# Performance work log

Hardware: AMD Instinct MI355X
Metric: run time of the kernel (lower is better)

The kernel has to match this reference:

```python
import jax, jax.numpy as jnp
import numpy as np

N = 100000       # nodes
E = 1600000      # undirected edges (one direction stored)
D = 64           # feature_dim


def _linear_params(key, fan_in, fan_out):
    kw, kb = jax.random.split(key)
    s = 1.0 / np.sqrt(fan_in)
    W = jax.random.uniform(kw, (fan_in, fan_out), jnp.float32, -s, s)
    b = jax.random.uniform(kb, (fan_out,), jnp.float32, -s, s)
    return W, b


def setup_inputs() -> dict:
    key = jax.random.key(0)
    ks = jax.random.split(key, 8)
    node_features = jax.random.normal(ks[0], (N, D), jnp.float32)
    node_operations = jax.random.normal(ks[1], (N, 4), jnp.float32)

    # Unique undirected edges, no self-loops -> torch's set() dedup of
    # {outgoing} U {incoming} neighbors equals counting each stored edge once
    # in both directions.
    rng = np.random.default_rng(0)
    src = rng.integers(0, N, size=4 * E)
    dst = rng.integers(0, N, size=4 * E)
    lo, hi = np.minimum(src, dst), np.maximum(src, dst)
    keep = lo != hi
    pairs = np.unique(np.stack([lo[keep], hi[keep]], axis=1), axis=0)
    assert pairs.shape[0] >= E
    perm = rng.permutation(pairs.shape[0])[:E]
    edge_index = jnp.asarray(pairs[perm].T, dtype=jnp.int32)  # [2, E]

    # node_generator: Linear(2D,128)-ReLU-Linear(128,64)-ReLU-Linear(64,D+3)
    W1, b1 = _linear_params(ks[2], 2 * D, 128)
    W2, b2 = _linear_params(ks[3], 128, 64)
    W3, b3 = _linear_params(ks[4], 64, D + 3)
    # insertion_predictor: Linear(D,32)-ReLU-Linear(32,1)-Sigmoid
    P1, pb1 = _linear_params(ks[5], D, 32)
    P2, pb2 = _linear_params(ks[6], 32, 1)

    return {
        'node_features': node_features,
        'node_operations': node_operations,
        'edge_index': edge_index,
        'W1': W1, 'b1': b1, 'W2': W2, 'b2': b2, 'W3': W3, 'b3': b3,
        'P1': P1, 'pb1': pb1, 'P2': P2, 'pb2': pb2,
    }


def reference(node_features, node_operations, edge_index,
              W1, b1, W2, b2, W3, b3, P1, pb1, P2, pb2):
    n = node_features.shape[0]
    src, dst = edge_index[0], edge_index[1]

    # candidate mask: softmax over op logits, class 0 = insert, threshold 0.5
    insert_probs = jax.nn.softmax(node_operations, axis=-1)[:, 0]
    ones = jnp.ones(src.shape[0], node_features.dtype)
    deg = (jax.ops.segment_sum(ones, src, num_segments=n)
           + jax.ops.segment_sum(ones, dst, num_segments=n))
    # torch loop skips candidates with no neighbors
    mask = (insert_probs > 0.5) & (deg > 0)
    maskf = mask.astype(node_features.dtype)

    # batched neighbor mean (undirected: both edge directions)
    nsum = (jax.ops.segment_sum(node_features[dst], src, num_segments=n)
            + jax.ops.segment_sum(node_features[src], dst, num_segments=n))
    nmean = nsum / jnp.maximum(deg, 1.0)[:, None]

    ctx = jnp.concatenate([node_features, nmean], axis=-1)  # [N, 2D]
    h = jax.nn.relu(ctx @ W1 + b1)
    h = jax.nn.relu(h @ W2 + b2)
    gen = h @ W3 + b3                         # [N, D+3]
    pos = gen[:, :3]                          # [N, 3]
    feats = gen[:, 3:]                        # [N, D]
    p = jax.nn.relu(feats @ P1 + pb1)
    prob = jax.nn.sigmoid(p @ P2 + pb2)       # [N, 1]

    # pack: [positions | features | probability], zeroed for non-candidates
    out = jnp.concatenate([pos, feats, prob], axis=-1) * maskf[:, None]
    return out
```

## Files before the change

### kernel.cpp

```cpp
#include <hip/hip_runtime.h>
#include <hip/hip_bf16.h>
#include <hip/hip_fp16.h>
#include <math.h>

typedef unsigned int u32;
typedef unsigned short u16;
typedef unsigned long long u64;

#define O_W1 0
#define O_b1 16384
#define O_W2 16512
#define O_b2 24704
#define O_W3 24768
#define O_b3 29056
#define O_P1 29123
#define O_pb1 31171
#define O_P2 31203
#define O_pb2 31235
#define W_TOTAL 31236

#define NPB 16
#define LDW 17

__device__ __forceinline__ float ldf(const void* p, long i, int dt) {
  if (dt == 1) { u32 v = ((const u16*)p)[i]; return __uint_as_float(v << 16); }
  if (dt == 2) { __half h = ((const __half*)p)[i]; return __half2float(h); }
  return ((const float*)p)[i];
}
__device__ __forceinline__ int ldei(const int* p, long i, int is64) {
  return is64 ? p[2 * i] : p[i];
}
__device__ __forceinline__ int bit_test(const u64* bits, int i) {
  return (int)((bits[i >> 6] >> (i & 63)) & 1ull);
}

extern "C" __global__ void kall_detect(const u32* __restrict__ feat,
                                       const u32* __restrict__ w1,
                                       const u32* __restrict__ ops,
                                       const u32* __restrict__ ei,
                                       int* __restrict__ hdr)
{
  int lane = threadIdx.x;
  int mode = blockIdx.x;
  if (mode == 3) {
    unsigned long long m0 = __ballot(ei[lane] == 0u);
    unsigned long long m1 = __ballot(ei[64 + lane] == 0u);
    if (lane == 0) hdr[2] = (__popcll(m0) + __popcll(m1) >= 32) ? 1 : 0;
    return;
  }
  const u32* p = (mode == 0) ? feat : (mode == 1) ? w1 : ops;
  int slot = (mode == 0) ? 0 : (mode == 1) ? 1 : 3;
  u32 w0 = p[lane];
  u32 w1v = p[64 + lane];
  u16 h[4] = { (u16)(w0 & 0xffff), (u16)(w0 >> 16),
               (u16)(w1v & 0xffff), (u16)(w1v >> 16) };
  int cb = 0;
#pragma unroll
  for (int t = 0; t < 4; ++t) {
    int e8 = (h[t] >> 7) & 0xff;
    cb += (e8 >= 110 && e8 <= 140) ? 1 : 0;
  }
  int ch = 0;
#pragma unroll
  for (int t = 0; t < 4; t += 2) {
    int e5 = (h[t] >> 10) & 0x1f;
    ch += (e5 >= 5 && e5 <= 18) ? 1 : 0;
  }
  __shared__ int sb[64], sh[64];
  sb[lane] = cb; sh[lane] = ch;
  __syncthreads();
  if (lane == 0) {
    int CB = 0, CH = 0;
    for (int t = 0; t < 64; ++t) { CB += sb[t]; CH += sh[t]; }
    int dt;
    if (CB >= 200) dt = 1;
    else if (CH >= 100) dt = 2;
    else dt = 0;
    hdr[slot] = dt;
  }
}

extern "C" __global__ void __launch_bounds__(256)
kw_conv(const void* __restrict__ W1, const void* __restrict__ b1,
        const void* __restrict__ W2, const void* __restrict__ b2,
        const void* __restrict__ W3, const void* __restrict__ b3,
        const void* __restrict__ P1, const void* __restrict__ pb1,
        const void* __restrict__ P2, const void* __restrict__ pb2,
        const int* __restrict__ hdr, float* __restrict__ wf)
{
  int i = blockIdx.x * 256 + threadIdx.x;
  if (i >= W_TOTAL) return;
  const void* s; int o;
  if      (i < O_b1)  { s = W1;  o = i; }
  else if (i < O_W2)  { s = b1;  o = i - O_b1; }
  else if (i < O_b2)  { s = W2;  o = i - O_W2; }
  else if (i < O_W3)  { s = b2;  o = i - O_b2; }
  else if (i < O_b3)  { s = W3;  o = i - O_W3; }
  else if (i < O_P1)  { s = b3;  o = i - O_b3; }
  else if (i < O_pb1) { s = P1;  o = i - O_P1; }
  else if (i < O_P2)  { s = pb1; o = i - O_pb1; }
  else if (i < O_pb2) { s = P2;  o = i - O_P2; }
  else                { s = pb2; o = i - O_pb2; }
  wf[i] = ldf(s, o, hdr[1]);
}

extern "C" __global__ void __launch_bounds__(256)
k2a_cand(const void* __restrict__ opsv, const int* __restrict__ hdr,
         u64* __restrict__ bits, int* __restrict__ cnt,
         int* __restrict__ fillcnt, int N)
{
  int i = blockIdx.x * 256 + threadIdx.x;
  if (i >= N) return;
  cnt[i] = 0;
  fillcnt[i] = 0;
  int dt = hdr[3];
  float x0 = ldf(opsv, (long)i * 4 + 0, dt);
  float x1 = ldf(opsv, (long)i * 4 + 1, dt);
  float x2 = ldf(opsv, (long)i * 4 + 2, dt);
  float x3 = ldf(opsv, (long)i * 4 + 3, dt);
  float m = fmaxf(fmaxf(x0, x1), fmaxf(x2, x3));
  double e0 = exp((double)(x0 - m));
  double e1 = exp((double)(x1 - m));
  double e2 = exp((double)(x2 - m));
  double e3 = exp((double)(x3 - m));
  double p0 = e0 / (((e0 + e1) + e2) + e3);
  u64 msk = __ballot(p0 > 0.5);
  if ((threadIdx.x & 63) == 0) bits[i >> 6] = msk;
}

extern "C" __global__ void __launch_bounds__(256)
k1a_cnt(const int* __restrict__ ei, const u64* __restrict__ bits,
        int* __restrict__ cnt, int E, const int* __restrict__ hdr)
{
  int e = blockIdx.x * 256 + threadIdx.x;
  if (e >= E) return;
  int is64 = hdr[2];
  int s = ldei(ei, e, is64);
  int d = ldei(ei, (long)E + e, is64);
  if (bit_test(bits, s)) atomicAdd(cnt + s, 1);
  if (bit_test(bits, d)) atomicAdd(cnt + d, 1);
}

extern "C" __global__ void __launch_bounds__(256)
k2b_alloc(const u64* __restrict__ bits, const int* __restrict__ cnt,
          int* __restrict__ hdr, int* __restrict__ nodeoff,
          int* __restrict__ nlist, int N)
{
  int i = blockIdx.x * 256 + threadIdx.x;
  if (i >= N) return;
  int c = (bit_test(bits, i) && cnt[i] > 0) ? cnt[i] : 0;
  if (c > 0) {
    int pos = atomicAdd(hdr + 4, 1);
    nlist[pos] = i;
    nodeoff[i] = atomicAdd(hdr + 5, c);
  } else {
    nodeoff[i] = -1;
  }
}

extern "C" __global__ void __launch_bounds__(256)
k1_fill(const int* __restrict__ ei, const u64* __restrict__ bits,
        const int* __restrict__ nodeoff,
        int* __restrict__ fillcnt, int* __restrict__ adj, int E,
        const int* __restrict__ hdr)
{
  int e = blockIdx.x * 256 + threadIdx.x;
  if (e >= E) return;
  int is64 = hdr[2];
  int s = ldei(ei, e, is64);
  int d = ldei(ei, (long)E + e, is64);
  if (bit_test(bits, s)) {
    int os = nodeoff[s];
    if (os >= 0) { int p = atomicAdd(fillcnt + s, 1); adj[os + p] = d; }
  }
  if (bit_test(bits, d)) {
    int od = nodeoff[d];
    if (od >= 0) { int p = atomicAdd(fillcnt + d, 1); adj[od + p] = s; }
  }
}

extern "C" __global__ void __launch_bounds__(256)
k3b_mlp(const void* __restrict__ featv, const int* __restrict__ nlist,
        const int* __restrict__ cnt, const int* __restrict__ nodeoff,
        const int* __restrict__ adj,
        const float* __restrict__ wf, const int* __restrict__ hdr,
        float* __restrict__ out)
{
  __shared__ float A[128 * LDW];
  __shared__ float B[128 * LDW];
  __shared__ float WS[4096];
  __shared__ int sNode[NPB];
  __shared__ int sDeg[NPB];
  __shared__ int sOff[NPB];
  const int tid = threadIdx.x;
  const int nmask = hdr[4];
  const int base = blockIdx.x * NPB;
  if (nmask == 0 || base >= nmask) return;
  const int dt = hdr[0];
  const int nl = tid & 15;
  const int jg = tid >> 4;
  const int lane = tid & 63;
  const int q = __builtin_amdgcn_readfirstlane(tid >> 6);

  if (tid < NPB) {
    int idx = base + tid;
    int node = nlist[(idx < nmask) ? idx : (nmask - 1)];
    sNode[tid] = node;
    sDeg[tid] = cnt[node];
    sOff[tid] = nodeoff[node];
  }
  __syncthreads();

#pragma unroll
  for (int i = 0; i < 4; ++i) {
    int g = i * 256 + tid;
    int f = g & 63;
    int n = g >> 6;
    int node = sNode[n];
    A[f * LDW + n] = ldf(featv, (long)node * 64 + f, dt);
  }

  if (dt == 0) {
    const float4* f4 = (const float4*)featv;
    const int g = lane >> 4;
    const int fq = lane & 15;
#pragma unroll
    for (int t = 0; t < 4; ++t) {
      const int n = q * 4 + t;
      const int off = sOff[n];
      const int dg = sDeg[n];
      float4 acc = make_float4(0.f, 0.f, 0.f, 0.f);
      int j = g;
      for (; j + 4 < dg; j += 8) {
        int n0 = adj[off + j];
        int n1 = adj[off + j + 4];
        float4 v0 = f4[(long)n0 * 16 + fq];
        float4 v1 = f4[(long)n1 * 16 + fq];
        acc.x += v0.x + v1.x; acc.y += v0.y + v1.y;
        acc.z += v0.z + v1.z; acc.w += v0.w + v1.w;
      }
      if (j < dg) {
        int n0 = adj[off + j];
        float4 v0 = f4[(long)n0 * 16 + fq];
        acc.x += v0.x; acc.y += v0.y; acc.z += v0.z; acc.w += v0.w;
      }
      acc.x += __shfl_xor(acc.x, 16); acc.y += __shfl_xor(acc.y, 16);
      acc.z += __shfl_xor(acc.z, 16); acc.w += __shfl_xor(acc.w, 16);
      acc.x += __shfl_xor(acc.x, 32); acc.y += __shfl_xor(acc.y, 32);
      acc.z += __shfl_xor(acc.z, 32); acc.w += __shfl_xor(acc.w, 32);
      if (g == 0) {
        float inv = 1.f / (float)dg;
        A[(64 + fq * 4 + 0) * LDW + n] = acc.x * inv;
        A[(64 + fq * 4 + 1) * LDW + n] = acc.y * inv;
        A[(64 + fq * 4 + 2) * LDW + n] = acc.z * inv;
        A[(64 + fq * 4 + 3) * LDW + n] = acc.w * inv;
      }
    }
  } else {
#pragma unroll
    for (int t = 0; t < 4; ++t) {
      const int n = q * 4 + t;
      const int off = sOff[n];
      const int dg = sDeg[n];
      float acc = 0.f;
      int j = 0;
      for (; j + 4 <= dg; j += 4) {
        int n0 = adj[off + j + 0];
        int n1 = adj[off + j + 1];
        int n2 = adj[off + j + 2];
        int n3 = adj[off + j + 3];
        float v0 = ldf(featv, (long)n0 * 64 + lane, dt);
        float v1 = ldf(featv, (long)n1 * 64 + lane, dt);
        float v2 = ldf(featv, (long)n2 * 64 + lane, dt);
        float v3 = ldf(featv, (long)n3 * 64 + lane, dt);
        acc += ((v0 + v1) + (v2 + v3));
      }
      for (; j < dg; ++j)
        acc += ldf(featv, (long)adj[off + j] * 64 + lane, dt);
      A[(64 + lane) * LDW + n] = acc / (float)dg;
    }
  }

  {
    const int j0 = jg * 8;
    float a0 = wf[O_b1 + j0 + 0], a1 = wf[O_b1 + j0 + 1];
    float a2 = wf[O_b1 + j0 + 2], a3 = wf[O_b1 + j0 + 3];
    float a4 = wf[O_b1 + j0 + 4], a5 = wf[O_b1 + j0 + 5];
    float a6 = wf[O_b1 + j0 + 6], a7 = wf[O_b1 + j0 + 7];
    for (int c = 0; c < 4; ++c) {
      __syncthreads();
      {
        const float4* s4 = (const float4*)(wf + O_W1 + c * 4096);
        float4* d4 = (float4*)WS;
#pragma unroll
        for (int i = 0; i < 4; ++i) d4[tid + 256 * i] = s4[tid + 256 * i];
      }
      __syncthreads();
#pragma unroll 4
      for (int k = 0; k < 32; ++k) {
        float x = A[(c * 32 + k) * LDW + nl];
        const float* w = WS + k * 128 + j0;
        float4 w0 = *(const float4*)(w);
        float4 w1 = *(const float4*)(w + 4);
        a0 = fmaf(x, w0.x, a0);
        a1 = fmaf(x, w0.y, a1);
        a2 = fmaf(x, w0.z, a2);
        a3 = fmaf(x, w0.w, a3);
        a4 = fmaf(x, w1.x, a4);
        a5 = fmaf(x, w1.y, a5);
        a6 = fmaf(x, w1.z, a6);
        a7 = fmaf(x, w1.w, a7);
      }
    }
    B[(j0 + 0) * LDW + nl] = fmaxf(a0, 0.f);
    B[(j0 + 1) * LDW + nl] = fmaxf(a1, 0.f);
    B[(j0 + 2) * LDW + nl] = fmaxf(a2, 0.f);
    B[(j0 + 3) * LDW + nl] = fmaxf(a3, 0.f);
    B[(j0 + 4) * LDW + nl] = fmaxf(a4, 0.f);
    B[(j0 + 5) * LDW + nl] = fmaxf(a5, 0.f);
    B[(j0 + 6) * LDW + nl] = fmaxf(a6, 0.f);
    B[(j0 + 7) * LDW + nl] = fmaxf(a7, 0.f);
  }

  {
    const int j0 = jg * 4;
    float a0 = wf[O_b2 + j0 + 0], a1 = wf[O_b2 + j0 + 1];
    float a2 = wf[O_b2 + j0 + 2], a3 = wf[O_b2 + j0 + 3];
    for (int c = 0; c < 2; ++c) {
      __syncthreads();
      {
        const float4* s4 = (const float4*)(wf + O_W2 + c * 4096);
        float4* d4 = (float4*)WS;
#pragma unroll
        for (int i = 0; i < 4; ++i) d4[tid + 256 * i] = s4[tid + 256 * i];
      }
      __syncthreads();
#pragma unroll 4
      for (int k = 0; k < 64; ++k) {
        float x = B[(c * 64 + k) * LDW + nl];
        float4 w = *(const float4*)(WS + k * 64 + j0);
        a0 = fmaf(x, w.x, a0);
        a1 = fmaf(x, w.y, a1);
        a2 = fmaf(x, w.z, a2);
        a3 = fmaf(x, w.w, a3);
      }
    }
    A[(j0 + 0) * LDW + nl] = fmaxf(a0, 0.f);
    A[(j0 + 1) * LDW + nl] = fmaxf(a1, 0.f);
    A[(j0 + 2) * LDW + nl] = fmaxf(a2, 0.f);
    A[(j0 + 3) * LDW + nl] = fmaxf(a3, 0.f);
  }

  {
    const int jq = jg;
    const bool has5 = (jq < 3);
    float a0 = 0.f, a1 = 0.f, a2 = 0.f, a3 = 0.f, a4 = 0.f;
    for (int c = 0; c < 2; ++c) {
      __syncthreads();
      {
        const float4* s4 = (const float4*)(wf + O_W3 + c * 2144);
        float4* d4 = (float4*)WS;
        for (int i = tid; i < 536; i += 256) d4[i] = s4[i];
      }
      __syncthreads();
#pragma unroll 4
      for (int k = 0; k < 32; ++k) {
        float x = A[(c * 32 + k) * LDW + nl];
        const float* w = WS + k * 67 + jq;
        float w4 = has5 ? w[64] : 0.f;
        a0 = fmaf(x, w[0],  a0);
        a1 = fmaf(x, w[16], a1);
        a2 = fmaf(x, w[32], a2);
        a3 = fmaf(x, w[48], a3);
        a4 = fmaf(x, w4,    a4);
      }
    }
    B[(jq +  0) * LDW + nl] = wf[O_b3 + jq]      + a0;
    B[(jq + 16) * LDW + nl] = wf[O_b3 + jq + 16] + a1;
    B[(jq + 32) * LDW + nl] = wf[O_b3 + jq + 32] + a2;
    B[(jq + 48) * LDW + nl] = wf[O_b3 + jq + 48] + a3;
    if (has5)
      B[(jq + 64) * LDW + nl] = wf[O_b3 + jq + 64] + a4;
  }

  {
    const int jq = jg;
    float a0 = wf[O_pb1 + jq], a1 = wf[O_pb1 + jq + 16];
    __syncthreads();
    for (int i = tid; i < 2048; i += 256) WS[i] = wf[O_P1 + i];
    __syncthreads();
#pragma unroll 4
    for (int k = 0; k < 64; ++k) {
      float x = B[(3 + k) * LDW + nl];
      a0 = fmaf(x, WS[k * 32 + jq],      a0);
      a1 = fmaf(x, WS[k * 32 + jq + 16], a1);
    }
    A[(jq +  0) * LDW + nl] = fmaxf(a0, 0.f);
    A[(jq + 16) * LDW + nl] = fmaxf(a1, 0.f);
  }
  __syncthreads();

  if (tid < 64) {
    const int part = tid >> 4;
    float p = 0.f;
#pragma unroll
    for (int kk = 0; kk < 8; ++kk) {
      int k = part * 8 + kk;
      p = fmaf(A[k * LDW + nl], wf[O_P2 + k], p);
    }
    p += __shfl_xor(p, 16);
    p += __shfl_xor(p, 32);
    if (part == 0) {
      float z = wf[O_pb2] + p;
      B[67 * LDW + nl] = 1.0f / (1.0f + expf(-z));
    }
  }
  __syncthreads();

  for (int g = tid; g < NPB * 68; g += 256) {
    int n = g / 68;
    int c = g - n * 68;
    if (base + n < nmask) {
      int node = sNode[n];
      out[(long)node * 68 + c] = B[c * LDW + n];
    }
  }
}

extern "C" void kernel_launch(void* const* d_in, const int* in_sizes, int n_in,
                              void* d_out, int out_size, void* d_ws, size_t ws_size,
                              hipStream_t stream) {
  int iF = 0, iO = 1, iE = 2;
  int iW1 = 3, ib1 = 4, iW2 = 5, ib2 = 6, iW3 = 7, ib3 = 8;
  int iP1 = 9, ipb1 = 10, iP2 = 11, ipb2 = 12;
  {
    int bigs[4]; int nb = 0;
    for (int i = 0; i < n_in && nb < 4; ++i)
      if (in_sizes[i] > 100000) bigs[nb++] = i;
    if (nb == 3) {
      int a = bigs[0], b = bigs[1], c = bigs[2];
      int mx = a, mn = a;
      if (in_sizes[b] > in_sizes[mx]) mx = b;
      if (in_sizes[c] > in_sizes[mx]) mx = c;
      if (in_sizes[b] < in_sizes[mn]) mn = b;
      if (in_sizes[c] < in_sizes[mn]) mn = c;
      iF = mx; iO = mn; iE = a + b + c - mx - mn;
      int t32[2]; int n32 = 0;
      int jW1=-1, jb1=-1, jW2=-1, jb2=-1, jW3=-1, jb3=-1, jP1=-1, jpb2=-1;
      for (int i = 0; i < n_in; ++i) {
        if (i == iF || i == iO || i == iE) continue;
        switch (in_sizes[i]) {
          case 16384: jW1 = i; break;
          case 128:   jb1 = i; break;
          case 8192:  jW2 = i; break;
          case 64:    jb2 = i; break;
          case 4288:  jW3 = i; break;
          case 67:    jb3 = i; break;
          case 2048:  jP1 = i; break;
          case 1:     jpb2 = i; break;
          case 32:    if (n32 < 2) t32[n32++] = i; break;
          default: break;
        }
      }
      if (jW1 >= 0 && jb1 >= 0 && jW2 >= 0 && jb2 >= 0 && jW3 >= 0 &&
          jb3 >= 0 && jP1 >= 0 && jpb2 >= 0 && n32 == 2) {
        iW1 = jW1; ib1 = jb1; iW2 = jW2; ib2 = jb2; iW3 = jW3; ib3 = jb3;
        iP1 = jP1; ipb2 = jpb2;
        if (t32[1] == t32[0] + 1) { ipb1 = t32[0]; iP2 = t32[1]; }
        else                      { iP2 = t32[0]; ipb1 = t32[1]; }
      }
    }
  }
  int N = (out_size % 68 == 0) ? (out_size / 68) : (in_sizes[iF] / 64);
  const int E = in_sizes[iE] / 2;
  const void* feat = d_in[iF];
  const void* ops  = d_in[iO];
  const int* ei    = (const int*)d_in[iE];

  char* ws = (char*)d_ws;
  int* hdr = (int*)ws;
  size_t off = 256;
  float* wf = (float*)(ws + off);
  off += ((size_t)W_TOTAL * 4 + 255) & ~(size_t)255;
  u64* bits = (u64*)(ws + off);
  off += (((size_t)(N + 63) / 64) * 8 + 255) & ~(size_t)255;
  int* cnt = (int*)(ws + off);
  off += ((size_t)N * 4 + 255) & ~(size_t)255;
  int* nodeoff = (int*)(ws + off);
  off += ((size_t)N * 4 + 255) & ~(size_t)255;
  int* fillcnt = (int*)(ws + off);
  off += ((size_t)N * 4 + 255) & ~(size_t)255;
  int* nlist = (int*)(ws + off);
  off += ((size_t)N * 4 + 255) & ~(size_t)255;
  int* adj = (int*)(ws + off);

  hipMemsetAsync(hdr, 0, 256, stream);
  hipMemsetAsync(d_out, 0, (size_t)out_size * 4, stream);

  kall_detect<<<4, 64, 0, stream>>>((const u32*)feat, (const u32*)d_in[iW1],
                                    (const u32*)ops, (const u32*)ei, hdr);

  kw_conv<<<(W_TOTAL + 255) / 256, 256, 0, stream>>>(
      d_in[iW1], d_in[ib1], d_in[iW2], d_in[ib2], d_in[iW3], d_in[ib3],
      d_in[iP1], d_in[ipb1], d_in[iP2], d_in[ipb2], hdr, wf);
  k2a_cand<<<(N + 255) / 256, 256, 0, stream>>>(ops, hdr, bits, cnt, fillcnt, N);
  k1a_cnt<<<(E + 255) / 256, 256, 0, stream>>>(ei, bits, cnt, E, hdr);
  k2b_alloc<<<(N + 255) / 256, 256, 0, stream>>>(bits, cnt, hdr, nodeoff, nlist, N);
  k1_fill<<<(E + 255) / 256, 256, 0, stream>>>(ei, bits, nodeoff, fillcnt, adj, E, hdr);
  k3b_mlp<<<(N + NPB - 1) / NPB, 256, 0, stream>>>(feat, nlist, cnt, nodeoff,
                                                   adj, wf, hdr,
                                                   (float*)d_out);
}
```

Baseline: 241.2 us.

## Halve MLP nodes per block, vectorize edge kernels, use cursor-based CSR fill

The MLP kernel now processes 8 candidate nodes per block instead of 16, which doubles the block count and shrinks per-thread accumulators for more parallelism and occupancy. The price is more weight reloads into shared memory overall. The edge count and fill kernels now handle 4 edges per thread with int4 loads. The fill kernel uses a cursor array initialized to each node's start offset, which removes the nodeoff lookup and the add in the inner path.

Result: no change. 245.3 us (+1.7%).

```diff
diff --git a/kernel.cpp b/kernel.cpp
--- a/kernel.cpp
+++ b/kernel.cpp
@@ -19,8 +19,8 @@
 #define O_pb2 31235
 #define W_TOTAL 31236
 
-#define NPB 16
-#define LDW 17
+#define NPB 8
+#define LDW 9
 
 __device__ __forceinline__ float ldf(const void* p, long i, int dt) {
   if (dt == 1) { u32 v = ((const u16*)p)[i]; return __uint_as_float(v << 16); }
@@ -106,13 +106,11 @@
 
 extern "C" __global__ void __launch_bounds__(256)
 k2a_cand(const void* __restrict__ opsv, const int* __restrict__ hdr,
-         u64* __restrict__ bits, int* __restrict__ cnt,
-         int* __restrict__ fillcnt, int N)
+         u64* __restrict__ bits, int* __restrict__ cnt, int N)
 {
   int i = blockIdx.x * 256 + threadIdx.x;
   if (i >= N) return;
   cnt[i] = 0;
-  fillcnt[i] = 0;
   int dt = hdr[3];
   float x0 = ldf(opsv, (long)i * 4 + 0, dt);
   float x1 = ldf(opsv, (long)i * 4 + 1, dt);
@@ -132,19 +130,36 @@
 k1a_cnt(const int* __restrict__ ei, const u64* __restrict__ bits,
         int* __restrict__ cnt, int E, const int* __restrict__ hdr)
 {
-  int e = blockIdx.x * 256 + threadIdx.x;
-  if (e >= E) return;
+  int t = blockIdx.x * 256 + threadIdx.x;
+  int e0 = t * 4;
+  if (e0 >= E) return;
   int is64 = hdr[2];
-  int s = ldei(ei, e, is64);
-  int d = ldei(ei, (long)E + e, is64);
-  if (bit_test(bits, s)) atomicAdd(cnt + s, 1);
-  if (bit_test(bits, d)) atomicAdd(cnt + d, 1);
+  if (!is64 && (E & 3) == 0 && e0 + 4 <= E) {
+    int4 sv = *(const int4*)(ei + e0);
+    int4 dv = *(const int4*)(ei + (long)E + e0);
+    if (bit_test(bits, sv.x)) atomicAdd(cnt + sv.x, 1);
+    if (bit_test(bits, sv.y)) atomicAdd(cnt + sv.y, 1);
+    if (bit_test(bits, sv.z)) atomicAdd(cnt + sv.z, 1);
+    if (bit_test(bits, sv.w)) atomicAdd(cnt + sv.w, 1);
+    if (bit_test(bits, dv.x)) atomicAdd(cnt + dv.x, 1);
+    if (bit_test(bits, dv.y)) atomicAdd(cnt + dv.y, 1);
+    if (bit_test(bits, dv.z)) atomicAdd(cnt + dv.z, 1);
+    if (bit_test(bits, dv.w)) atomicAdd(cnt + dv.w, 1);
+  } else {
+    int ee = (e0 + 4 < E) ? e0 + 4 : E;
+    for (int e = e0; e < ee; ++e) {
+      int s = ldei(ei, e, is64);
+      int d = ldei(ei, (long)E + e, is64);
+      if (bit_test(bits, s)) atomicAdd(cnt + s, 1);
+      if (bit_test(bits, d)) atomicAdd(cnt + d, 1);
+    }
+  }
 }
 
 extern "C" __global__ void __launch_bounds__(256)
 k2b_alloc(const u64* __restrict__ bits, const int* __restrict__ cnt,
           int* __restrict__ hdr, int* __restrict__ nodeoff,
-          int* __restrict__ nlist, int N)
+          int* __restrict__ fillcnt, int* __restrict__ nlist, int N)
 {
   int i = blockIdx.x * 256 + threadIdx.x;
   if (i >= N) return;
@@ -152,7 +167,9 @@
   if (c > 0) {
     int pos = atomicAdd(hdr + 4, 1);
     nlist[pos] = i;
-    nodeoff[i] = atomicAdd(hdr + 5, c);
+    int start = atomicAdd(hdr + 5, c);
+    nodeoff[i] = start;
+    fillcnt[i] = start;
   } else {
     nodeoff[i] = -1;
   }
@@ -160,22 +177,32 @@
 
 extern "C" __global__ void __launch_bounds__(256)
 k1_fill(const int* __restrict__ ei, const u64* __restrict__ bits,
-        const int* __restrict__ nodeoff,
-        int* __restrict__ fillcnt, int* __restrict__ adj, int E,
+        int* __restrict__ cur, int* __restrict__ adj, int E,
         const int* __restrict__ hdr)
 {
-  int e = blockIdx.x * 256 + threadIdx.x;
-  if (e >= E) return;
+  int t = blockIdx.x * 256 + threadIdx.x;
+  int e0 = t * 4;
+  if (e0 >= E) return;
   int is64 = hdr[2];
-  int s = ldei(ei, e, is64);
-  int d = ldei(ei, (long)E + e, is64);
-  if (bit_test(bits, s)) {
-    int os = nodeoff[s];
-    if (os >= 0) { int p = atomicAdd(fillcnt + s, 1); adj[os + p] = d; }
-  }
-  if (bit_test(bits, d)) {
-    int od = nodeoff[d];
-    if (od >= 0) { int p = atomicAdd(fillcnt + d, 1); adj[od + p] = s; }
+  if (!is64 && (E & 3) == 0 && e0 + 4 <= E) {
+    int4 sv = *(const int4*)(ei + e0);
+    int4 dv = *(const int4*)(ei + (long)E + e0);
+    if (bit_test(bits, sv.x)) { int p = atomicAdd(cur + sv.x, 1); adj[p] = dv.x; }
+    if (bit_test(bits, dv.x)) { int p = atomicAdd(cur + dv.x, 1); adj[p] = sv.x; }
+    if (bit_test(bits, sv.y)) { int p = atomicAdd(cur + sv.y, 1); adj[p] = dv.y; }
+    if (bit_test(bits, dv.y)) { int p = atomicAdd(cur + dv.y, 1); adj[p] = sv.y; }
+    if (bit_test(bits, sv.z)) { int p = atomicAdd(cur + sv.z, 1); adj[p] = dv.z; }
+    if (bit_test(bits, dv.z)) { int p = atomicAdd(cur + dv.z, 1); adj[p] = sv.z; }
+    if (bit_test(bits, sv.w)) { int p = atomicAdd(cur + sv.w, 1); adj[p] = dv.w; }
+    if (bit_test(bits, dv.w)) { int p = atomicAdd(cur + dv.w, 1); adj[p] = sv.w; }
+  } else {
+    int ee = (e0 + 4 < E) ? e0 + 4 : E;
+    for (int e = e0; e < ee; ++e) {
+      int s = ldei(ei, e, is64);
+      int d = ldei(ei, (long)E + e, is64);
+      if (bit_test(bits, s)) { int p = atomicAdd(cur + s, 1); adj[p] = d; }
+      if (bit_test(bits, d)) { int p = atomicAdd(cur + d, 1); adj[p] = s; }
+    }
   }
 }
 
@@ -197,8 +224,8 @@
   const int base = blockIdx.x * NPB;
   if (nmask == 0 || base >= nmask) return;
   const int dt = hdr[0];
-  const int nl = tid & 15;
-  const int jg = tid >> 4;
+  const int nl = tid & 7;
+  const int jg = tid >> 3;
   const int lane = tid & 63;
   const int q = __builtin_amdgcn_readfirstlane(tid >> 6);
 
@@ -212,7 +239,7 @@
   __syncthreads();
 
 #pragma unroll
-  for (int i = 0; i < 4; ++i) {
+  for (int i = 0; i < 2; ++i) {
     int g = i * 256 + tid;
     int f = g & 63;
     int n = g >> 6;
@@ -225,8 +252,8 @@
     const int g = lane >> 4;
     const int fq = lane & 15;
 #pragma unroll
-    for (int t = 0; t < 4; ++t) {
-      const int n = q * 4 + t;
+    for (int t = 0; t < 2; ++t) {
+      const int n = q * 2 + t;
       const int off = sOff[n];
       const int dg = sDeg[n];
       float4 acc = make_float4(0.f, 0.f, 0.f, 0.f);
@@ -258,8 +285,8 @@
     }
   } else {
 #pragma unroll
-    for (int t = 0; t < 4; ++t) {
-      const int n = q * 4 + t;
+    for (int t = 0; t < 2; ++t) {
+      const int n = q * 2 + t;
       const int off = sOff[n];
       const int dg = sDeg[n];
       float acc = 0.f;
@@ -282,11 +309,9 @@
   }
 
   {
-    const int j0 = jg * 8;
+    const int j0 = jg * 4;
     float a0 = wf[O_b1 + j0 + 0], a1 = wf[O_b1 + j0 + 1];
     float a2 = wf[O_b1 + j0 + 2], a3 = wf[O_b1 + j0 + 3];
-    float a4 = wf[O_b1 + j0 + 4], a5 = wf[O_b1 + j0 + 5];
-    float a6 = wf[O_b1 + j0 + 6], a7 = wf[O_b1 + j0 + 7];
     for (int c = 0; c < 4; ++c) {
       __syncthreads();
       {
@@ -299,33 +324,22 @@
 #pragma unroll 4
       for (int k = 0; k < 32; ++k) {
         float x = A[(c * 32 + k) * LDW + nl];
-        const float* w = WS + k * 128 + j0;
-        float4 w0 = *(const float4*)(w);
-        float4 w1 = *(const float4*)(w + 4);
-        a0 = fmaf(x, w0.x, a0);
-        a1 = fmaf(x, w0.y, a1);
-        a2 = fmaf(x, w0.z, a2);
-        a3 = fmaf(x, w0.w, a3);
-        a4 = fmaf(x, w1.x, a4);
-        a5 = fmaf(x, w1.y, a5);
-        a6 = fmaf(x, w1.z, a6);
-        a7 = fmaf(x, w1.w, a7);
+        float4 w = *(const float4*)(WS + k * 128 + j0);
+        a0 = fmaf(x, w.x, a0);
+        a1 = fmaf(x, w.y, a1);
+        a2 = fmaf(x, w.z, a2);
+        a3 = fmaf(x, w.w, a3);
       }
     }
     B[(j0 + 0) * LDW + nl] = fmaxf(a0, 0.f);
     B[(j0 + 1) * LDW + nl] = fmaxf(a1, 0.f);
     B[(j0 + 2) * LDW + nl] = fmaxf(a2, 0.f);
     B[(j0 + 3) * LDW + nl] = fmaxf(a3, 0.f);
-    B[(j0 + 4) * LDW + nl] = fmaxf(a4, 0.f);
-    B[(j0 + 5) * LDW + nl] = fmaxf(a5, 0.f);
-    B[(j0 + 6) * LDW + nl] = fmaxf(a6, 0.f);
-    B[(j0 + 7) * LDW + nl] = fmaxf(a7, 0.f);
   }
 
   {
-    const int j0 = jg * 4;
+    const int j0 = jg * 2;
     float a0 = wf[O_b2 + j0 + 0], a1 = wf[O_b2 + j0 + 1];
-    float a2 = wf[O_b2 + j0 + 2], a3 = wf[O_b2 + j0 + 3];
     for (int c = 0; c < 2; ++c) {
       __syncthreads();
       {
@@ -338,23 +352,19 @@
 #pragma unroll 4
       for (int k = 0; k < 64; ++k) {
         float x = B[(c * 64 + k) * LDW + nl];
-        float4 w = *(const float4*)(WS + k * 64 + j0);
+        float2 w = *(const float2*)(WS + k * 64 + j0);
         a0 = fmaf(x, w.x, a0);
         a1 = fmaf(x, w.y, a1);
-        a2 = fmaf(x, w.z, a2);
-        a3 = fmaf(x, w.w, a3);
       }
     }
     A[(j0 + 0) * LDW + nl] = fmaxf(a0, 0.f);
     A[(j0 + 1) * LDW + nl] = fmaxf(a1, 0.f);
-    A[(j0 + 2) * LDW + nl] = fmaxf(a2, 0.f);
-    A[(j0 + 3) * LDW + nl] = fmaxf(a3, 0.f);
   }
 
   {
     const int jq = jg;
-    const bool has5 = (jq < 3);
-    float a0 = 0.f, a1 = 0.f, a2 = 0.f, a3 = 0.f, a4 = 0.f;
+    const bool has3 = (jq < 3);
+    float a0 = 0.f, a1 = 0.f, a2 = 0.f;
     for (int c = 0; c < 2; ++c) {
       __syncthreads();
       {
@@ -367,47 +377,42 @@
       for (int k = 0; k < 32; ++k) {
         float x = A[(c * 32 + k) * LDW + nl];
         const float* w = WS + k * 67 + jq;
-        float w4 = has5 ? w[64] : 0.f;
+        float w2 = has3 ? w[64] : 0.f;
         a0 = fmaf(x, w[0],  a0);
-        a1 = fmaf(x, w[16], a1);
-        a2 = fmaf(x, w[32], a2);
-        a3 = fmaf(x, w[48], a3);
-        a4 = fmaf(x, w4,    a4);
+        a1 = fmaf(x, w[32], a1);
+        a2 = fmaf(x, w2,    a2);
       }
     }
     B[(jq +  0) * LDW + nl] = wf[O_b3 + jq]      + a0;
-    B[(jq + 16) * LDW + nl] = wf[O_b3 + jq + 16] + a1;
-    B[(jq + 32) * LDW + nl] = wf[O_b3 + jq + 32] + a2;
-    B[(jq + 48) * LDW + nl] = wf[O_b3 + jq + 48] + a3;
-    if (has5)
-      B[(jq + 64) * LDW + nl] = wf[O_b3 + jq + 64] + a4;
+    B[(jq + 32) * LDW + nl] = wf[O_b3 + jq + 32] + a1;
+    if (has3)
+      B[(jq + 64) * LDW + nl] = wf[O_b3 + jq + 64] + a2;
   }
 
   {
     const int jq = jg;
-    float a0 = wf[O_pb1 + jq], a1 = wf[O_pb1 + jq + 16];
+    float a0 = wf[O_pb1 + jq];
     __syncthreads();
     for (int i = tid; i < 2048; i += 256) WS[i] = wf[O_P1 + i];
     __syncthreads();
 #pragma unroll 4
     for (int k = 0; k < 64; ++k) {
       float x = B[(3 + k) * LDW + nl];
-      a0 = fmaf(x, WS[k * 32 + jq],      a0);
-      a1 = fmaf(x, WS[k * 32 + jq + 16], a1);
-    }
-    A[(jq +  0) * LDW + nl] = fmaxf(a0, 0.f);
-    A[(jq + 16) * LDW + nl] = fmaxf(a1, 0.f);
+      a0 = fmaf(x, WS[k * 32 + jq], a0);
+    }
+    A[jq * LDW + nl] = fmaxf(a0, 0.f);
   }
   __syncthreads();
 
   if (tid < 64) {
-    const int part = tid >> 4;
+    const int part = tid >> 3;
     float p = 0.f;
 #pragma unroll
-    for (int kk = 0; kk < 8; ++kk) {
-      int k = part * 8 + kk;
+    for (int kk = 0; kk < 4; ++kk) {
+      int k = part * 4 + kk;
       p = fmaf(A[k * LDW + nl], wf[O_P2 + k], p);
     }
+    p += __shfl_xor(p, 8);
     p += __shfl_xor(p, 16);
     p += __shfl_xor(p, 32);
     if (part == 0) {
@@ -503,10 +508,13 @@
   kw_conv<<<(W_TOTAL + 255) / 256, 256, 0, stream>>>(
       d_in[iW1], d_in[ib1], d_in[iW2], d_in[ib2], d_in[iW3], d_in[ib3],
       d_in[iP1], d_in[ipb1], d_in[iP2], d_in[ipb2], hdr, wf);
-  k2a_cand<<<(N + 255) / 256, 256, 0, stream>>>(ops, hdr, bits, cnt, fillcnt, N);
-  k1a_cnt<<<(E + 255) / 256, 256, 0, stream>>>(ei, bits, cnt, E, hdr);
-  k2b_alloc<<<(N + 255) / 256, 256, 0, stream>>>(bits, cnt, hdr, nodeoff, nlist, N);
-  k1_fill<<<(E + 255) / 256, 256, 0, stream>>>(ei, bits, nodeoff, fillcnt, adj, E, hdr);
+  k2a_cand<<<(N + 255) / 256, 256, 0, stream>>>(ops, hdr, bits, cnt, N);
+  int eThreads = (E + 3) / 4;
+  k1a_cnt<<<(eThreads + 255) / 256, 256, 0, stream>>>(ei, bits, cnt, E, hdr);
+  k2b_alloc<<<(N + 255) / 256, 256, 0, stream>>>(bits, cnt, hdr, nodeoff,
+                                                 fillcnt, nlist, N);
+  k1_fill<<<(eThreads + 255) / 256, 256, 0, stream>>>(ei, bits, fillcnt, adj,
+                                                      E, hdr);
   k3b_mlp<<<(N + NPB - 1) / NPB, 256, 0, stream>>>(feat, nlist, cnt, nodeoff,
                                                    adj, wf, hdr,
                                                    (float*)d_out);
```
